# Performance work log

Hardware: AMD Instinct MI355X
Metric: run time of the kernel (lower is better)

## Reference

```python
import jax, jax.numpy as jnp
import numpy as np
import math

T_KER = 1.0
SIGMA = 0.1
COVAR = 5
EPS = 1e-6


def cos_kernel(a, b):
    # a:[B,N,D], b:[B,M,D] -> exp((cos_sim - 1)/T)
    num = jnp.einsum('bnd,bmd->bnm', a, b)
    den = jnp.linalg.norm(a, axis=-1)[..., None] * jnp.linalg.norm(b, axis=-1)[:, None] + EPS
    return jnp.exp((num / den - 1.0) / T_KER)


def get_local_cov(cov, K):
    # cov: [b,h,w,h,w] -> local KxK windows around the diagonal: [b,h,w,K*K]
    b, h, w = cov.shape[0], cov.shape[1], cov.shape[2]
    hw = h * w
    pad = K // 2
    covp = jnp.pad(cov, ((0, 0), (0, 0), (0, 0), (pad, pad), (pad, pad)))
    covp = covp.reshape(b, hw, h + K - 1, w + K - 1)
    dr, dc = np.meshgrid(np.arange(-pad, pad + 1), np.arange(-pad, pad + 1), indexing='ij')
    rb, cb = np.meshgrid(np.arange(pad, pad + h), np.arange(pad, pad + w), indexing='ij')
    rows = (rb[:, :, None, None] + dr[None, None]).reshape(hw, K * K)
    cols = (cb[:, :, None, None] + dc[None, None]).reshape(hw, K * K)
    pts = np.broadcast_to(np.arange(hw)[:, None], (hw, K * K))
    local = covp[:, pts, rows, cols]  # [b,hw,K*K]
    return local.reshape(b, h, w, K * K)


def reference(x, y, pos_w, pos_b):
    b, c, h1, w1 = x.shape
    h2, w2 = y.shape[2], y.shape[3]
    n2 = h2 * w2
    # positional encoding (fourier basis on [-1,1] grid)
    ys = jnp.linspace(-1 + 1 / h2, 1 - 1 / h2, h2)
    xs = jnp.linspace(-1 + 1 / w2, 1 - 1 / w2, w2)
    gy, gx = jnp.meshgrid(ys, xs, indexing='ij')
    coords = jnp.stack([gx, gy], axis=0)  # [2,h2,w2], (x,y) order
    f = jnp.cos(8 * math.pi * (jnp.einsum('dc,chw->dhw', pos_w, coords) + pos_b[:, None, None]))
    d = f.shape[0]
    xf = x.transpose(0, 2, 3, 1).reshape(b, h1 * w1, c)
    yf = y.transpose(0, 2, 3, 1).reshape(b, n2, c)
    ff = jnp.broadcast_to(f.transpose(1, 2, 0).reshape(1, n2, d), (b, n2, d))
    K_yy = cos_kernel(yf, yf)
    K_xy = cos_kernel(xf, yf)
    K_yy_plus = K_yy + SIGMA * jnp.eye(n2, dtype=K_yy.dtype)[None]
    I = jnp.broadcast_to(jnp.eye(n2, dtype=K_yy.dtype), (b, n2, n2))
    K_yy_inv = jnp.linalg.solve(K_yy_plus, I)
    mu = K_xy @ (K_yy_inv @ ff)  # [b, h1*w1, d]
    mu_x = mu.reshape(b, h1, w1, d).transpose(0, 3, 1, 2)
    K_xx = cos_kernel(xf, xf)
    cov = K_xx - K_xy @ (K_yy_inv @ jnp.swapaxes(K_xy, 1, 2))
    cov = cov.reshape(b, h1, w1, h1, w1)
    local = get_local_cov(cov, COVAR).transpose(0, 3, 1, 2)  # [b,K*K,h1,w1]
    return jnp.concatenate([mu_x, local], axis=1)


def setup_inputs() -> dict:
    key = jax.random.key(0)
    k0, k1, k2, k3 = jax.random.split(key, 4)
    return {
        'x': jax.random.normal(k0, (2, 512, 64, 64), dtype=jnp.float32),
        'y': jax.random.normal(k1, (2, 512, 64, 64), dtype=jnp.float32),
        'pos_w': jax.random.normal(k2, (64, 2), dtype=jnp.float32) * 0.5,
        'pos_b': jax.random.normal(k3, (64,), dtype=jnp.float32) * 0.1,
    }
```

## Files before the change

### kernel.cpp

```cpp
#include <hip/hip_runtime.h>
#include <math.h>

#define NPT 4096
#define CCH 512
#define NB 64
#define NKB 64
#define LDB 4160
#define SIGF 0.1f
#define CEPS 1e-6f
#define PI8 25.132741228718345f

#define APSTR ((size_t)2080 * 4096)
#define ILSTR ((size_t)64 * 4096)

typedef __attribute__((ext_vector_type(8))) short bf16x8;
typedef __attribute__((ext_vector_type(4))) float f32x4;
typedef __attribute__((ext_vector_type(4))) unsigned short us4;
typedef unsigned short ushort_t;

__device__ __forceinline__ size_t tbase(int I, int J) {
    return ((size_t)((I * (I + 1) >> 1) + J)) << 12;
}

__device__ inline ushort_t f2bf_rne(float x) {
    unsigned u = __float_as_uint(x);
    unsigned r = u + 0x7FFFu + ((u >> 16) & 1u);
    return (ushort_t)(r >> 16);
}
__device__ inline float bf2f(ushort_t h) { return __uint_as_float(((unsigned)h) << 16); }

__device__ inline void split4(float4 v, us4& h, us4& l) {
    h[0] = f2bf_rne(v.x); l[0] = f2bf_rne(v.x - bf2f(h[0]));
    h[1] = f2bf_rne(v.y); l[1] = f2bf_rne(v.y - bf2f(h[1]));
    h[2] = f2bf_rne(v.z); l[2] = f2bf_rne(v.z - bf2f(h[2]));
    h[3] = f2bf_rne(v.w); l[3] = f2bf_rne(v.w - bf2f(h[3]));
}

__global__ __launch_bounds__(256) void norms_kernel(const float* __restrict__ X,
                                                    float* __restrict__ nrm, int bofs) {
    int slot = blockIdx.y;
    int p = blockIdx.x * 256 + threadIdx.x;
    const float* Xb = X + (size_t)(slot + bofs) * CCH * NPT;
    float s = 0.f;
    #pragma unroll 8
    for (int ch = 0; ch < CCH; ++ch) {
        float v = Xb[(size_t)ch * NPT + p];
        s += v * v;
    }
    nrm[slot * NPT + p] = sqrtf(s);
}

__global__ __launch_bounds__(256) void split_kernel(const float* __restrict__ X,
                                                    ushort_t* __restrict__ Hi,
                                                    ushort_t* __restrict__ Lo,
                                                    int bofs) {
    int ch0 = blockIdx.x * 64, pt0 = blockIdx.y * 64;
    const float* Xb = X + (size_t)bofs * CCH * NPT;
    __shared__ float ls[64][65];
    int tid = threadIdx.x;
    for (int t = tid; t < 4096; t += 256) {
        int chl = t >> 6, ptl = t & 63;
        ls[chl][ptl] = Xb[(size_t)(ch0 + chl) * NPT + pt0 + ptl];
    }
    __syncthreads();
    for (int t = tid; t < 4096; t += 256) {
        int ptl = t >> 6, chl = t & 63;
        float v = ls[chl][ptl];
        ushort_t h = f2bf_rne(v);
        float lo = v - bf2f(h);
        Hi[(size_t)(pt0 + ptl) * CCH + ch0 + chl] = h;
        Lo[(size_t)(pt0 + ptl) * CCH + ch0 + chl] = f2bf_rne(lo);
    }
}

__global__ __launch_bounds__(256) void gramA_packed_kernel(
    const ushort_t* __restrict__ Yhi, const ushort_t* __restrict__ Ylo,
    const float* __restrict__ nY, float* __restrict__ Cp)
{
    int bx = blockIdx.x, by = blockIdx.y;
    if (bx > by) return;
    int bm = by * 128, bn = bx * 128;

    __shared__ __align__(16) ushort_t Ah[128][40];
    __shared__ __align__(16) ushort_t Al[128][40];
    __shared__ __align__(16) ushort_t Bh[128][40];
    __shared__ __align__(16) ushort_t Bl[128][40];

    int tid = threadIdx.x;
    int lane = tid & 63, wid = tid >> 6;
    int wr = wid >> 1, wc = wid & 1;

    f32x4 acc[4][4];
    #pragma unroll
    for (int i = 0; i < 4; ++i)
        #pragma unroll
        for (int j = 0; j < 4; ++j) acc[i][j] = (f32x4){0.f, 0.f, 0.f, 0.f};

    int arr = tid >> 6;
    int srow = lane >> 2, sc4 = lane & 3;
    const ushort_t* src = (arr == 0 || arr == 2) ? Yhi : Ylo;
    int pbase = (arr < 2) ? bm : bn;
    ushort_t* dst = (arr == 0) ? &Ah[0][0] : (arr == 1) ? &Al[0][0] : (arr == 2) ? &Bh[0][0] : &Bl[0][0];

    for (int k0 = 0; k0 < CCH; k0 += 32) {
        #pragma unroll
        for (int it = 0; it < 8; ++it) {
            int row = it * 16 + srow;
            const ushort_t* g = src + (size_t)(pbase + row) * CCH + k0 + sc4 * 8;
            bf16x8 v = *(const bf16x8*)g;
            *(bf16x8*)(dst + row * 40 + sc4 * 8) = v;
        }
        __syncthreads();
        bf16x8 afh[4], afl[4], bfh[4], bfl[4];
        int kcol = (lane >> 4) * 8;
        #pragma unroll
        for (int mi = 0; mi < 4; ++mi) {
            int r = wr * 64 + mi * 16 + (lane & 15);
            afh[mi] = *(const bf16x8*)&Ah[r][kcol];
            afl[mi] = *(const bf16x8*)&Al[r][kcol];
        }
        #pragma unroll
        for (int nj = 0; nj < 4; ++nj) {
            int r = wc * 64 + nj * 16 + (lane & 15);
            bfh[nj] = *(const bf16x8*)&Bh[r][kcol];
            bfl[nj] = *(const bf16x8*)&Bl[r][kcol];
        }
        #pragma unroll
        for (int mi = 0; mi < 4; ++mi)
            #pragma unroll
            for (int nj = 0; nj < 4; ++nj) {
                acc[mi][nj] = __builtin_amdgcn_mfma_f32_16x16x32_bf16(afh[mi], bfh[nj], acc[mi][nj], 0, 0, 0);
                acc[mi][nj] = __builtin_amdgcn_mfma_f32_16x16x32_bf16(afh[mi], bfl[nj], acc[mi][nj], 0, 0, 0);
                acc[mi][nj] = __builtin_amdgcn_mfma_f32_16x16x32_bf16(afl[mi], bfh[nj], acc[mi][nj], 0, 0, 0);
            }
        __syncthreads();
    }

    int I = (bm >> 6) + wr, J = (bn >> 6) + wc;
    if (J > I) return;
    float* Ct = Cp + tbase(I, J);
    #pragma unroll
    for (int nj = 0; nj < 4; ++nj) {
        int cin = nj * 16 + (lane & 15);
        float nbv = nY[bn + wc * 64 + cin];
        #pragma unroll
        for (int mi = 0; mi < 4; ++mi) {
            f32x4 a = acc[mi][nj];
            #pragma unroll
            for (int q = 0; q < 4; ++q) {
                int rin = mi * 16 + (lane >> 4) * 4 + q;
                float den = nY[bm + wr * 64 + rin] * nbv + CEPS;
                float v = expf(a[q] / den - 1.0f);
                if (I == J && rin == cin) v += SIGF;
                Ct[(rin << 6) + cin] = v;
            }
        }
    }
}

__global__ __launch_bounds__(256) void gramX_kernel(
    const ushort_t* __restrict__ Yhi, const ushort_t* __restrict__ Ylo,
    const float* __restrict__ Xf,
    const float* __restrict__ nY, const float* __restrict__ nX,
    float* __restrict__ Cm)
{
    int bm = blockIdx.y * 128, bn = blockIdx.x * 128;

    __shared__ __align__(16) ushort_t Ah[128][40];
    __shared__ __align__(16) ushort_t Al[128][40];
    __shared__ __align__(16) ushort_t Bh[128][40];
    __shared__ __align__(16) ushort_t Bl[128][40];

    int tid = threadIdx.x;
    int lane = tid & 63, wid = tid >> 6;
    int wr = wid >> 1, wc = wid & 1;

    f32x4 acc[4][4];
    #pragma unroll
    for (int i = 0; i < 4; ++i)
        #pragma unroll
        for (int j = 0; j < 4; ++j) acc[i][j] = (f32x4){0.f, 0.f, 0.f, 0.f};

    int srow = lane >> 2, sc4 = lane & 3;

    for (int k0 = 0; k0 < CCH; k0 += 32) {
        if (tid < 128) {
            const ushort_t* src = (tid < 64) ? Yhi : Ylo;
            ushort_t* dst = (tid < 64) ? &Ah[0][0] : &Al[0][0];
            #pragma unroll
            for (int it = 0; it < 8; ++it) {
                int row = it * 16 + srow;
                bf16x8 v = *(const bf16x8*)(src + (size_t)(bm + row) * CCH + k0 + sc4 * 8);
                *(bf16x8*)(dst + row * 40 + sc4 * 8) = v;
            }
        } else {
            int e0 = (tid - 128) * 8;
            #pragma unroll
            for (int i = 0; i < 8; ++i) {
                int e = e0 + i;
                int ch = e >> 5, p4 = e & 31;
                float4 v = *(const float4*)&Xf[(size_t)(k0 + ch) * NPT + bn + (p4 << 2)];
                us4 h, l;
                split4(v, h, l);
                #pragma unroll
                for (int q = 0; q < 4; ++q) {
                    Bh[(p4 << 2) + q][ch] = h[q];
                    Bl[(p4 << 2) + q][ch] = l[q];
                }
            }
        }
        __syncthreads();
        bf16x8 afh[4], afl[4], bfh[4], bfl[4];
        int kcol = (lane >> 4) * 8;
        #pragma unroll
        for (int mi = 0; mi < 4; ++mi) {
            int r = wr * 64 + mi * 16 + (lane & 15);
            afh[mi] = *(const bf16x8*)&Ah[r][kcol];
            afl[mi] = *(const bf16x8*)&Al[r][kcol];
        }
        #pragma unroll
        for (int nj = 0; nj < 4; ++nj) {
            int r = wc * 64 + nj * 16 + (lane & 15);
            bfh[nj] = *(const bf16x8*)&Bh[r][kcol];
            bfl[nj] = *(const bf16x8*)&Bl[r][kcol];
        }
        #pragma unroll
        for (int mi = 0; mi < 4; ++mi)
            #pragma unroll
            for (int nj = 0; nj < 4; ++nj) {
                acc[mi][nj] = __builtin_amdgcn_mfma_f32_16x16x32_bf16(afh[mi], bfh[nj], acc[mi][nj], 0, 0, 0);
                acc[mi][nj] = __builtin_amdgcn_mfma_f32_16x16x32_bf16(afh[mi], bfl[nj], acc[mi][nj], 0, 0, 0);
                acc[mi][nj] = __builtin_amdgcn_mfma_f32_16x16x32_bf16(afl[mi], bfh[nj], acc[mi][nj], 0, 0, 0);
            }
        __syncthreads();
    }

    #pragma unroll
    for (int nj = 0; nj < 4; ++nj) {
        int col = bn + wc * 64 + nj * 16 + (lane & 15);
        float nbv = nX[col];
        #pragma unroll
        for (int mi = 0; mi < 4; ++mi) {
            f32x4 a = acc[mi][nj];
            #pragma unroll
            for (int q = 0; q < 4; ++q) {
                int row = bm + wr * 64 + mi * 16 + (lane >> 4) * 4 + q;
                float den = nY[row] * nbv + CEPS;
                Cm[(size_t)row * LDB + col] = expf(a[q] / den - 1.0f);
            }
        }
    }
}

__global__ __launch_bounds__(256) void features_kernel(const float* __restrict__ pw,
                                                       const float* __restrict__ pb,
                                                       float* __restrict__ Brhs) {
    int g = blockIdx.x * 256 + threadIdx.x;
    int q = g >> 6, dd = g & 63;
    int hh = q >> 6, ww = q & 63;
    float gy = -1.0f + (2 * hh + 1) / 64.0f;
    float gx = -1.0f + (2 * ww + 1) / 64.0f;
    float ph = PI8 * (pw[dd * 2 + 0] * gx + pw[dd * 2 + 1] * gy + pb[dd]);
    Brhs[(size_t)q * LDB + NPT + dd] = cosf(ph);
}

__global__ __launch_bounds__(256) void potf2_packed_kernel(float* __restrict__ AmatP,
                                                           float* __restrict__ invL, int kb) {
    __shared__ float a[NB][NB + 4];
    __shared__ float iv[NB][NB + 4];
    __shared__ float ddiag[NB];
    int slot = blockIdx.z;
    float* Ab = AmatP + (size_t)slot * APSTR + tbase(kb, kb);
    int tid = threadIdx.x;
    int tx = tid & 15, ty = tid >> 4;
    for (int t = tid; t < NB * NB; t += 256) {
        int i = t >> 6, j = t & 63;
        a[i][j] = Ab[(i << 6) + j];
        iv[i][j] = 0.0f;
    }
    __syncthreads();
    for (int j = 0; j < NB; ++j) {
        float ajj = sqrtf(a[j][j]);
        float dinv = 1.0f / ajj;
        if (tid == 0) ddiag[j] = ajj;
        for (int i = j + 1 + tid; i < NB; i += 256) a[i][j] *= dinv;
        for (int c = tid; c <= j; c += 256)
            iv[j][c] = ((c == j ? 1.0f : 0.0f) - iv[j][c]) * dinv;
        __syncthreads();
        for (int i = j + 1 + ty; i < NB; i += 16) {
            float lij = a[i][j];
            for (int jj = j + 1 + tx; jj < NB; jj += 16)
                a[i][jj] -= lij * a[jj][j];
            for (int c = tx; c <= j; c += 16)
                iv[i][c] += lij * iv[j][c];
        }
        __syncthreads();
    }
    float* iL = invL + (size_t)slot * ILSTR + ((size_t)kb << 12);
    for (int t = tid; t < NB * NB; t += 256) {
        int i = t >> 6, j = t & 63;
        if (j < i)       Ab[(i << 6) + j] = a[i][j];
        else if (j == i) Ab[(i << 6) + j] = ddiag[i];
        iL[t] = (j <= i) ? iv[i][j] : 0.0f;
    }
}

__global__ __launch_bounds__(256) void trsm_packed_kernel(float* __restrict__ AmatP,
                                                          const float* __restrict__ invL, int kb) {
    int slot = blockIdx.z;
    int I = kb + 1 + blockIdx.x;
    float* At = AmatP + (size_t)slot * APSTR + tbase(I, kb);
    const float* iL = invL + (size_t)slot * ILSTR + ((size_t)kb << 12);

    __shared__ __align__(16) ushort_t Aoh[64][72], Aol[64][72];
    __shared__ __align__(16) ushort_t Bh[64][72], Bl[64][72];

    int tid = threadIdx.x, lane = tid & 63, w = tid >> 6;
    int frow = lane & 15, fk = (lane >> 4) << 3;
    f32x4 acc[4];
    #pragma unroll
    for (int j = 0; j < 4; ++j) acc[j] = (f32x4){0, 0, 0, 0};

    for (int e = tid; e < 1024; e += 256) {
        int r = e >> 4, k4 = e & 15;
        us4 h, l;
        float4 v = *(const float4*)&At[(r << 6) + (k4 << 2)];
        split4(v, h, l);
        *(us4*)&Aoh[r][k4 << 2] = h; *(us4*)&Aol[r][k4 << 2] = l;
        float4 u = *(const float4*)&iL[(r << 6) + (k4 << 2)];
        split4(u, h, l);
        *(us4*)&Bh[r][k4 << 2] = h; *(us4*)&Bl[r][k4 << 2] = l;
    }
    __syncthreads();
    #pragma unroll
    for (int kk0 = 0; kk0 < 64; kk0 += 32) {
        bf16x8 ah = *(const bf16x8*)&Aoh[(w << 4) + frow][kk0 + fk];
        bf16x8 al = *(const bf16x8*)&Aol[(w << 4) + frow][kk0 + fk];
        #pragma unroll
        for (int nj = 0; nj < 4; ++nj) {
            bf16x8 bh = *(const bf16x8*)&Bh[(nj << 4) + frow][kk0 + fk];
            bf16x8 bl = *(const bf16x8*)&Bl[(nj << 4) + frow][kk0 + fk];
            acc[nj] = __builtin_amdgcn_mfma_f32_16x16x32_bf16(ah, bh, acc[nj], 0, 0, 0);
            acc[nj] = __builtin_amdgcn_mfma_f32_16x16x32_bf16(ah, bl, acc[nj], 0, 0, 0);
            acc[nj] = __builtin_amdgcn_mfma_f32_16x16x32_bf16(al, bh, acc[nj], 0, 0, 0);
        }
    }
    #pragma unroll
    for (int nj = 0; nj < 4; ++nj)
        #pragma unroll
        for (int q = 0; q < 4; ++q) {
            int rin = (w << 4) + ((lane >> 4) << 2) + q;
            At[(rin << 6) + (nj << 4) + frow] = acc[nj][q];
        }
}

__global__ __launch_bounds__(256) void syrk_fact_packed_kernel(float* __restrict__ AmatP,
                                                               float* __restrict__ invL, int kb) {
    int bi = blockIdx.y, bj = blockIdx.x;
    if (bj > bi) return;
    int slot = blockIdx.z;
    int I = kb + 1 + bi, J = kb + 1 + bj;
    float* base = AmatP + (size_t)slot * APSTR;
    const float* Pi_t = base + tbase(I, kb);
    const float* Pj_t = base + tbase(J, kb);
    float* Ct = base + tbase(I, J);

    __shared__ __align__(16) char smem[36864];
    ushort_t (*Pih)[72] = (ushort_t(*)[72])(smem);
    ushort_t (*Pil)[72] = (ushort_t(*)[72])(smem + 9216);
    ushort_t (*Pjh)[72] = (ushort_t(*)[72])(smem + 18432);
    ushort_t (*Pjl)[72] = (ushort_t(*)[72])(smem + 27648);
    float (*fa)[68] = (float(*)[68])(smem);
    float (*fiv)[68] = (float(*)[68])(smem + 17408);
    float* fdd = (float*)(smem + 34816);

    int tid = threadIdx.x, lane = tid & 63, w = tid >> 6;
    int frow = lane & 15, fk = (lane >> 4) << 3;
    f32x4 acc[4];
    #pragma unroll
    for (int j = 0; j < 4; ++j) acc[j] = (f32x4){0, 0, 0, 0};

    for (int e = tid; e < 1024; e += 256) {
        int r = e >> 4, k4 = e & 15;
        us4 h, l;
        float4 v = *(const float4*)&Pi_t[(r << 6) + (k4 << 2)];
        split4(v, h, l);
        *(us4*)&Pih[r][k4 << 2] = h; *(us4*)&Pil[r][k4 << 2] = l;
        float4 u = *(const float4*)&Pj_t[(r << 6) + (k4 << 2)];
        split4(u, h, l);
        *(us4*)&Pjh[r][k4 << 2] = h; *(us4*)&Pjl[r][k4 << 2] = l;
    }
    __syncthreads();
    #pragma unroll
    for (int kk0 = 0; kk0 < 64; kk0 += 32) {
        bf16x8 ah = *(const bf16x8*)&Pih[(w << 4) + frow][kk0 + fk];
        bf16x8 al = *(const bf16x8*)&Pil[(w << 4) + frow][kk0 + fk];
        #pragma unroll
        for (int nj = 0; nj < 4; ++nj) {
            bf16x8 bh = *(const bf16x8*)&Pjh[(nj << 4) + frow][kk0 + fk];
            bf16x8 bl = *(const bf16x8*)&Pjl[(nj << 4) + frow][kk0 + fk];
            acc[nj] = __builtin_amdgcn_mfma_f32_16x16x32_bf16(ah, bh, acc[nj], 0, 0, 0);
            acc[nj] = __builtin_amdgcn_mfma_f32_16x16x32_bf16(ah, bl, acc[nj], 0, 0, 0);
            acc[nj] = __builtin_amdgcn_mfma_f32_16x16x32_bf16(al, bh, acc[nj], 0, 0, 0);
        }
    }

    if (!(bi == 0 && bj == 0)) {
        #pragma unroll
        for (int nj = 0; nj < 4; ++nj) {
            int cin = (nj << 4) + frow;
            #pragma unroll
            for (int q = 0; q < 4; ++q) {
                int rin = (w << 4) + ((lane >> 4) << 2) + q;
                Ct[(rin << 6) + cin] -= acc[nj][q];
            }
        }
        return;
    }

    __syncthreads();
    #pragma unroll
    for (int nj = 0; nj < 4; ++nj) {
        int cin = (nj << 4) + frow;
        #pragma unroll
        for (int q = 0; q < 4; ++q) {
            int rin = (w << 4) + ((lane >> 4) << 2) + q;
            fa[rin][cin] = Ct[(rin << 6) + cin] - acc[nj][q];
            fiv[rin][cin] = 0.0f;
        }
    }
    __syncthreads();
    int tx = tid & 15, ty = tid >> 4;
    for (int j = 0; j < NB; ++j) {
        float ajj = sqrtf(fa[j][j]);
        float dinv = 1.0f / ajj;
        if (tid == 0) fdd[j] = ajj;
        for (int i = j + 1 + tid; i < NB; i += 256) fa[i][j] *= dinv;
        for (int c = tid; c <= j; c += 256)
            fiv[j][c] = ((c == j ? 1.0f : 0.0f) - fiv[j][c]) * dinv;
        __syncthreads();
        for (int i = j + 1 + ty; i < NB; i += 16) {
            float lij = fa[i][j];
            for (int jj = j + 1 + tx; jj < NB; jj += 16)
                fa[i][jj] -= lij * fa[jj][j];
            for (int c = tx; c <= j; c += 16)
                fiv[i][c] += lij * fiv[j][c];
        }
        __syncthreads();
    }
    float* iL = invL + (size_t)slot * ILSTR + ((size_t)(kb + 1) << 12);
    for (int t = tid; t < NB * NB; t += 256) {
        int i = t >> 6, j = t & 63;
        if (j < i)       Ct[(i << 6) + j] = fa[i][j];
        else if (j == i) Ct[(i << 6) + j] = fdd[i];
        iL[t] = (j <= i) ? fiv[i][j] : 0.0f;
    }
}

__global__ __launch_bounds__(256) void trsm_rhs_kernel(float* __restrict__ Brhs,
                                                       const float* __restrict__ invL) {
    int n0 = blockIdx.x * 64;
    __shared__ float invLs[64][68];
    __shared__ float Tds[64][68];
    int tid = threadIdx.x;
    for (int e = tid; e < 1024; e += 256) {
        int r = e >> 4, k4 = e & 15;
        float4 v = *(const float4*)&Brhs[(size_t)r * LDB + n0 + (k4 << 2)];
        int c = k4 << 2;
        Tds[r][c] = v.x; Tds[r][c + 1] = v.y; Tds[r][c + 2] = v.z; Tds[r][c + 3] = v.w;
        float4 u = *(const float4*)&invL[(r << 6) + (k4 << 2)];
        invLs[r][c] = u.x; invLs[r][c + 1] = u.y; invLs[r][c + 2] = u.z; invLs[r][c + 3] = u.w;
    }
    __syncthreads();
    int col = tid & 63, rg = tid >> 6;
    #pragma unroll
    for (int i = 0; i < 16; ++i) {
        int r = (i << 2) + rg;
        float s = 0.f;
        #pragma unroll 16
        for (int k = 0; k < 64; ++k) s += invLs[r][k] * Tds[k][col];
        Brhs[(size_t)r * LDB + n0 + col] = s;
    }
}

__global__ __launch_bounds__(256) void solve_step_kernel(const float* __restrict__ AmatP,
                                                         float* __restrict__ Brhs,
                                                         const float* __restrict__ invL, int kb) {
    int n0 = blockIdx.x * 64;
    int I = kb + 1 + blockIdx.y;
    int rb = kb * NB;
    int ri = I * NB;
    const float* Lt = AmatP + tbase(I, kb);

    __shared__ __align__(16) char smem[36864];
    ushort_t (*Lh)[72] = (ushort_t(*)[72])(smem);
    ushort_t (*Ll)[72] = (ushort_t(*)[72])(smem + 9216);
    ushort_t (*Uh)[72] = (ushort_t(*)[72])(smem + 18432);
    ushort_t (*Ul)[72] = (ushort_t(*)[72])(smem + 27648);
    float (*invLs)[68] = (float(*)[68])(smem);
    float (*Tds)[68]   = (float(*)[68])(smem + 18432);

    int tid = threadIdx.x, lane = tid & 63, w = tid >> 6;
    int frow = lane & 15, fk = (lane >> 4) << 3;

    for (int e = tid; e < 1024; e += 256) {
        int r = e >> 4, k4 = e & 15;
        us4 h, l;
        float4 v = *(const float4*)&Lt[(r << 6) + (k4 << 2)];
        split4(v, h, l);
        *(us4*)&Lh[r][k4 << 2] = h; *(us4*)&Ll[r][k4 << 2] = l;
        float4 u = *(const float4*)&Brhs[(size_t)(rb + r) * LDB + n0 + (k4 << 2)];
        split4(u, h, l);
        #pragma unroll
        for (int q = 0; q < 4; ++q) {
            Uh[(k4 << 2) + q][r] = h[q];
            Ul[(k4 << 2) + q][r] = l[q];
        }
    }
    __syncthreads();

    f32x4 acc[4];
    #pragma unroll
    for (int j = 0; j < 4; ++j) acc[j] = (f32x4){0, 0, 0, 0};
    #pragma unroll
    for (int kk0 = 0; kk0 < 64; kk0 += 32) {
        bf16x8 ah = *(const bf16x8*)&Lh[(w << 4) + frow][kk0 + fk];
        bf16x8 al = *(const bf16x8*)&Ll[(w << 4) + frow][kk0 + fk];
        #pragma unroll
        for (int nj = 0; nj < 4; ++nj) {
            bf16x8 bh = *(const bf16x8*)&Uh[(nj << 4) + frow][kk0 + fk];
            bf16x8 bl = *(const bf16x8*)&Ul[(nj << 4) + frow][kk0 + fk];
            acc[nj] = __builtin_amdgcn_mfma_f32_16x16x32_bf16(ah, bh, acc[nj], 0, 0, 0);
            acc[nj] = __builtin_amdgcn_mfma_f32_16x16x32_bf16(ah, bl, acc[nj], 0, 0, 0);
            acc[nj] = __builtin_amdgcn_mfma_f32_16x16x32_bf16(al, bh, acc[nj], 0, 0, 0);
        }
    }

    if (blockIdx.y > 0) {
        #pragma unroll
        for (int nj = 0; nj < 4; ++nj) {
            int cin = (nj << 4) + frow;
            #pragma unroll
            for (int q = 0; q < 4; ++q) {
                int rin = (w << 4) + ((lane >> 4) << 2) + q;
                Brhs[(size_t)(ri + rin) * LDB + n0 + cin] -= acc[nj][q];
            }
        }
        return;
    }

    __syncthreads();
    #pragma unroll
    for (int nj = 0; nj < 4; ++nj) {
        int cin = (nj << 4) + frow;
        #pragma unroll
        for (int q = 0; q < 4; ++q) {
            int rin = (w << 4) + ((lane >> 4) << 2) + q;
            Tds[rin][cin] = Brhs[(size_t)(ri + rin) * LDB + n0 + cin] - acc[nj][q];
        }
    }
    const float* iL = invL + ((size_t)(kb + 1) << 12);
    for (int e = tid; e < 1024; e += 256) {
        int r = e >> 4, k4 = e & 15;
        float4 u = *(const float4*)&iL[(r << 6) + (k4 << 2)];
        int c = k4 << 2;
        invLs[r][c] = u.x; invLs[r][c + 1] = u.y; invLs[r][c + 2] = u.z; invLs[r][c + 3] = u.w;
    }
    __syncthreads();
    int col = tid & 63, rg = tid >> 6;
    #pragma unroll
    for (int i = 0; i < 16; ++i) {
        int r = (i << 2) + rg;
        float s = 0.f;
        #pragma unroll 16
        for (int k = 0; k < 64; ++k) s += invLs[r][k] * Tds[k][col];
        Brhs[(size_t)(ri + r) * LDB + n0 + col] = s;
    }
}

__global__ __launch_bounds__(256) void mu_kernel(const float* __restrict__ Brhs,
                                                 float* __restrict__ out, int bofs) {
    const float* Bb = Brhs;
    int p0 = blockIdx.x * 64;
    __shared__ float Us[16][65];
    __shared__ float Vs[16][65];
    float acc[4][4] = {};
    int tid = threadIdx.x, tx = tid & 15, ty = tid >> 4;
    for (int q0 = 0; q0 < NPT; q0 += 16) {
        for (int t = tid; t < 1024; t += 256) {
            int kk = t >> 6, c = t & 63;
            Us[kk][c] = Bb[(size_t)(q0 + kk) * LDB + p0 + c];
            Vs[kk][c] = Bb[(size_t)(q0 + kk) * LDB + NPT + c];
        }
        __syncthreads();
        #pragma unroll
        for (int kk = 0; kk < 16; ++kk) {
            float uv[4], vv[4];
            #pragma unroll
            for (int i = 0; i < 4; ++i) { uv[i] = Us[kk][ty * 4 + i]; vv[i] = Vs[kk][tx * 4 + i]; }
            #pragma unroll
            for (int i = 0; i < 4; ++i)
                #pragma unroll
                for (int j = 0; j < 4; ++j) acc[i][j] += uv[i] * vv[j];
        }
        __syncthreads();
    }
    #pragma unroll
    for (int i = 0; i < 4; ++i)
        #pragma unroll
        for (int j = 0; j < 4; ++j)
            out[((size_t)bofs * 89 + tx * 4 + j) * NPT + p0 + ty * 4 + i] = acc[i][j];
}

__global__ __launch_bounds__(256) void kxx_local_kernel(const float* __restrict__ X,
                                                        const float* __restrict__ nxb,
                                                        float* __restrict__ tmp, int bofs) {
    int r = blockIdx.y;
    int c0 = blockIdx.x * 16;
    const float* Xb = X + (size_t)bofs * CCH * NPT;
    __shared__ float Xs[32][104];
    int tid = threadIdx.x;
    int t0 = tid, t1 = tid + 256;
    int pl0 = t0 / 25, jj0 = t0 % 25;
    int pl1 = t1 / 25, jj1 = t1 % 25;
    int pidx0 = 40 + pl0 + 2;
    int jidx0 = (jj0 / 5) * 20 + pl0 + (jj0 % 5);
    int pidx1 = 40 + pl1 + 2;
    int jidx1 = (jj1 / 5) * 20 + pl1 + (jj1 % 5);
    float acc0 = 0.f, acc1 = 0.f;
    for (int ch0 = 0; ch0 < CCH; ch0 += 32) {
        for (int t = tid; t < 32 * 100; t += 256) {
            int ch = t / 100, i = t % 100;
            int s = i / 20, cc = i % 20;
            int gr = r + s - 2, gc = c0 - 2 + cc;
            float v = 0.f;
            if (gr >= 0 && gr < 64 && gc >= 0 && gc < 64)
                v = Xb[(size_t)(ch0 + ch) * NPT + gr * 64 + gc];
            Xs[ch][i] = v;
        }
        __syncthreads();
        #pragma unroll 8
        for (int kk = 0; kk < 32; ++kk) {
            acc0 += Xs[kk][pidx0] * Xs[kk][jidx0];
            if (t1 < 400) acc1 += Xs[kk][pidx1] * Xs[kk][jidx1];
        }
        __syncthreads();
    }
    {
        int p = r * 64 + c0 + pl0;
        int qr = r + jj0 / 5 - 2, qc = c0 + pl0 + jj0 % 5 - 2;
        float v = 0.f;
        if (qr >= 0 && qr < 64 && qc >= 0 && qc < 64) {
            int q = qr * 64 + qc;
            v = expf(acc0 / (nxb[p] * nxb[q] + CEPS) - 1.0f);
        }
        tmp[(size_t)jj0 * NPT + p] = v;
    }
    if (t1 < 400) {
        int p = r * 64 + c0 + pl1;
        int qr = r + jj1 / 5 - 2, qc = c0 + pl1 + jj1 % 5 - 2;
        float v = 0.f;
        if (qr >= 0 && qr < 64 && qc >= 0 && qc < 64) {
            int q = qr * 64 + qc;
            v = expf(acc1 / (nxb[p] * nxb[q] + CEPS) - 1.0f);
        }
        tmp[(size_t)jj1 * NPT + p] = v;
    }
}

__global__ __launch_bounds__(256) void cov_local_kernel(const float* __restrict__ Brhs,
                                                        const float* __restrict__ tmp,
                                                        float* __restrict__ out, int bofs) {
    int r = blockIdx.y;
    int c0 = blockIdx.x * 16;
    const float* Ub = Brhs;
    __shared__ float Us[64][104];
    int tid = threadIdx.x;
    int t0 = tid, t1 = tid + 256;
    int pl0 = t0 / 25, jj0 = t0 % 25;
    int pl1 = t1 / 25, jj1 = t1 % 25;
    int pidx0 = 40 + pl0 + 2;
    int jidx0 = (jj0 / 5) * 20 + pl0 + (jj0 % 5);
    int pidx1 = 40 + pl1 + 2;
    int jidx1 = (jj1 / 5) * 20 + pl1 + (jj1 % 5);
    float acc0 = 0.f, acc1 = 0.f;
    for (int q0 = 0; q0 < NPT; q0 += 64) {
        for (int t = tid; t < 64 * 100; t += 256) {
            int qq = t / 100, i = t % 100;
            int s = i / 20, cc = i % 20;
            int gr = r + s - 2, gc = c0 - 2 + cc;
            float v = 0.f;
            if (gr >= 0 && gr < 64 && gc >= 0 && gc < 64)
                v = Ub[(size_t)(q0 + qq) * LDB + gr * 64 + gc];
            Us[qq][i] = v;
        }
        __syncthreads();
        #pragma unroll 8
        for (int kk = 0; kk < 64; ++kk) {
            acc0 += Us[kk][pidx0] * Us[kk][jidx0];
            if (t1 < 400) acc1 += Us[kk][pidx1] * Us[kk][jidx1];
        }
        __syncthreads();
    }
    {
        int p = r * 64 + c0 + pl0;
        int qr = r + jj0 / 5 - 2, qc = c0 + pl0 + jj0 % 5 - 2;
        float v = 0.f;
        if (qr >= 0 && qr < 64 && qc >= 0 && qc < 64)
            v = tmp[(size_t)jj0 * NPT + p] - acc0;
        out[((size_t)bofs * 89 + 64 + jj0) * NPT + p] = v;
    }
    if (t1 < 400) {
        int p = r * 64 + c0 + pl1;
        int qr = r + jj1 / 5 - 2, qc = c0 + pl1 + jj1 % 5 - 2;
        float v = 0.f;
        if (qr >= 0 && qr < 64 && qc >= 0 && qc < 64)
            v = tmp[(size_t)jj1 * NPT + p] - acc1;
        out[((size_t)bofs * 89 + 64 + jj1) * NPT + p] = v;
    }
}

extern "C" void kernel_launch(void* const* d_in, const int* in_sizes, int n_in,
                              void* d_out, int out_size, void* d_ws, size_t ws_size,
                              hipStream_t stream) {
    (void)in_sizes; (void)n_in; (void)out_size;
    const float* x  = (const float*)d_in[0];
    const float* y  = (const float*)d_in[1];
    const float* pw = (const float*)d_in[2];
    const float* pb = (const float*)d_in[3];
    float* out = (float*)d_out;
    float* ws  = (float*)d_ws;

    const size_t NEED = 2 * APSTR + (size_t)NPT * LDB + 2 * ILSTR + 4 * NPT + 2 * ((size_t)NPT * CCH / 2);
    if (ws_size < NEED * sizeof(float)) return;

    float* AmatP = ws;
    float* Brhs  = AmatP + 2 * APSTR;
    float* invL  = Brhs + (size_t)NPT * LDB;
    float* nx    = invL + 2 * ILSTR;
    float* ny    = nx + 2 * NPT;
    float* ysBuf = ny + 2 * NPT;
    ushort_t* ysH = (ushort_t*)ysBuf;
    ushort_t* ysL = ysH + (size_t)NPT * CCH;
    float* tmp = invL;

    norms_kernel<<<dim3(16, 2), 256, 0, stream>>>(x, nx, 0);
    norms_kernel<<<dim3(16, 2), 256, 0, stream>>>(y, ny, 0);

    for (int b = 0; b < 2; ++b) {
        split_kernel<<<dim3(8, 64, 1), 256, 0, stream>>>(y, ysH, ysL, b);
        gramA_packed_kernel<<<dim3(32, 32, 1), 256, 0, stream>>>(
            ysH, ysL, ny + (size_t)b * NPT, AmatP + (size_t)b * APSTR);
    }

    potf2_packed_kernel<<<dim3(1, 1, 2), 256, 0, stream>>>(AmatP, invL, 0);
    for (int kb = 0; kb < NKB - 1; ++kb) {
        int nt = NKB - 1 - kb;
        trsm_packed_kernel<<<dim3(nt, 1, 2), 256, 0, stream>>>(AmatP, invL, kb);
        syrk_fact_packed_kernel<<<dim3(nt, nt, 2), 256, 0, stream>>>(AmatP, invL, kb);
    }

    for (int b = 0; b < 2; ++b) {
        split_kernel<<<dim3(8, 64, 1), 256, 0, stream>>>(y, ysH, ysL, b);
        features_kernel<<<dim3(1024, 1), 256, 0, stream>>>(pw, pb, Brhs);
        gramX_kernel<<<dim3(32, 32, 1), 256, 0, stream>>>(
            ysH, ysL, x + (size_t)b * CCH * NPT, ny + (size_t)b * NPT, nx + (size_t)b * NPT, Brhs);

        trsm_rhs_kernel<<<dim3(65, 1, 1), 256, 0, stream>>>(Brhs, invL + (size_t)b * ILSTR);
        for (int kb = 0; kb < NKB - 1; ++kb) {
            solve_step_kernel<<<dim3(65, NKB - 1 - kb, 1), 256, 0, stream>>>(
                AmatP + (size_t)b * APSTR, Brhs, invL + (size_t)b * ILSTR, kb);
        }

        mu_kernel<<<dim3(64, 1, 1), 256, 0, stream>>>(Brhs, out, b);
        kxx_local_kernel<<<dim3(4, 64, 1), 256, 0, stream>>>(x, nx + (size_t)b * NPT, tmp, b);
        cov_local_kernel<<<dim3(4, 64, 1), 256, 0, stream>>>(Brhs, tmp, out, b);
    }
}
```

Before: 11.39 ms.

## Batch triangular solves across both batches and split local covariance reduction

```diff
diff --git a/kernel.cpp b/kernel.cpp
--- a/kernel.cpp
+++ b/kernel.cpp
@@ -106,8 +106,7 @@
         #pragma unroll
         for (int it = 0; it < 8; ++it) {
             int row = it * 16 + srow;
-            const ushort_t* g = src + (size_t)(pbase + row) * CCH + k0 + sc4 * 8;
-            bf16x8 v = *(const bf16x8*)g;
+            bf16x8 v = *(const bf16x8*)(src + (size_t)(pbase + row) * CCH + k0 + sc4 * 8);
             *(bf16x8*)(dst + row * 40 + sc4 * 8) = v;
         }
         __syncthreads();
@@ -458,17 +457,21 @@
 }
 
 __global__ __launch_bounds__(256) void trsm_rhs_kernel(float* __restrict__ Brhs,
-                                                       const float* __restrict__ invL) {
+                                                       const float* __restrict__ invL,
+                                                       size_t brStride) {
+    int slot = blockIdx.z;
+    float* Bb = Brhs + (size_t)slot * brStride;
+    const float* iL = invL + (size_t)slot * ILSTR;
     int n0 = blockIdx.x * 64;
     __shared__ float invLs[64][68];
     __shared__ float Tds[64][68];
     int tid = threadIdx.x;
     for (int e = tid; e < 1024; e += 256) {
         int r = e >> 4, k4 = e & 15;
-        float4 v = *(const float4*)&Brhs[(size_t)r * LDB + n0 + (k4 << 2)];
+        float4 v = *(const float4*)&Bb[(size_t)r * LDB + n0 + (k4 << 2)];
         int c = k4 << 2;
         Tds[r][c] = v.x; Tds[r][c + 1] = v.y; Tds[r][c + 2] = v.z; Tds[r][c + 3] = v.w;
-        float4 u = *(const float4*)&invL[(r << 6) + (k4 << 2)];
+        float4 u = *(const float4*)&iL[(r << 6) + (k4 << 2)];
         invLs[r][c] = u.x; invLs[r][c + 1] = u.y; invLs[r][c + 2] = u.z; invLs[r][c + 3] = u.w;
     }
     __syncthreads();
@@ -479,18 +482,22 @@
         float s = 0.f;
         #pragma unroll 16
         for (int k = 0; k < 64; ++k) s += invLs[r][k] * Tds[k][col];
-        Brhs[(size_t)r * LDB + n0 + col] = s;
+        Bb[(size_t)r * LDB + n0 + col] = s;
     }
 }
 
 __global__ __launch_bounds__(256) void solve_step_kernel(const float* __restrict__ AmatP,
                                                          float* __restrict__ Brhs,
-                                                         const float* __restrict__ invL, int kb) {
+                                                         const float* __restrict__ invL,
+                                                         size_t brStride, int kb) {
+    int slot = blockIdx.z;
     int n0 = blockIdx.x * 64;
     int I = kb + 1 + blockIdx.y;
     int rb = kb * NB;
     int ri = I * NB;
-    const float* Lt = AmatP + tbase(I, kb);
+    const float* Lt = AmatP + (size_t)slot * APSTR + tbase(I, kb);
+    const float* iLbase = invL + (size_t)slot * ILSTR;
+    float* Bb = Brhs + (size_t)slot * brStride;
 
     __shared__ __align__(16) char smem[36864];
     ushort_t (*Lh)[72] = (ushort_t(*)[72])(smem);
@@ -509,7 +516,7 @@
         float4 v = *(const float4*)&Lt[(r << 6) + (k4 << 2)];
         split4(v, h, l);
         *(us4*)&Lh[r][k4 << 2] = h; *(us4*)&Ll[r][k4 << 2] = l;
-        float4 u = *(const float4*)&Brhs[(size_t)(rb + r) * LDB + n0 + (k4 << 2)];
+        float4 u = *(const float4*)&Bb[(size_t)(rb + r) * LDB + n0 + (k4 << 2)];
         split4(u, h, l);
         #pragma unroll
         for (int q = 0; q < 4; ++q) {
@@ -543,7 +550,7 @@
             #pragma unroll
             for (int q = 0; q < 4; ++q) {
                 int rin = (w << 4) + ((lane >> 4) << 2) + q;
-                Brhs[(size_t)(ri + rin) * LDB + n0 + cin] -= acc[nj][q];
+                Bb[(size_t)(ri + rin) * LDB + n0 + cin] -= acc[nj][q];
             }
         }
         return;
@@ -556,13 +563,13 @@
         #pragma unroll
         for (int q = 0; q < 4; ++q) {
             int rin = (w << 4) + ((lane >> 4) << 2) + q;
-            Tds[rin][cin] = Brhs[(size_t)(ri + rin) * LDB + n0 + cin] - acc[nj][q];
-        }
-    }
-    const float* iL = invL + ((size_t)(kb + 1) << 12);
+            Tds[rin][cin] = Bb[(size_t)(ri + rin) * LDB + n0 + cin] - acc[nj][q];
+        }
+    }
+    const float* iL2 = iLbase + ((size_t)(kb + 1) << 12);
     for (int e = tid; e < 1024; e += 256) {
         int r = e >> 4, k4 = e & 15;
-        float4 u = *(const float4*)&iL[(r << 6) + (k4 << 2)];
+        float4 u = *(const float4*)&iL2[(r << 6) + (k4 << 2)];
         int c = k4 << 2;
         invLs[r][c] = u.x; invLs[r][c + 1] = u.y; invLs[r][c + 2] = u.z; invLs[r][c + 3] = u.w;
     }
@@ -574,7 +581,7 @@
         float s = 0.f;
         #pragma unroll 16
         for (int k = 0; k < 64; ++k) s += invLs[r][k] * Tds[k][col];
-        Brhs[(size_t)(ri + r) * LDB + n0 + col] = s;
+        Bb[(size_t)(ri + r) * LDB + n0 + col] = s;
     }
 }
 
@@ -610,6 +617,11 @@
         #pragma unroll
         for (int j = 0; j < 4; ++j)
             out[((size_t)bofs * 89 + tx * 4 + j) * NPT + p0 + ty * 4 + i] = acc[i][j];
+}
+
+__global__ __launch_bounds__(256) void zero_kernel(float* __restrict__ p, int n) {
+    int i = blockIdx.x * 256 + threadIdx.x;
+    if (i < n) p[i] = 0.0f;
 }
 
 __global__ __launch_bounds__(256) void kxx_local_kernel(const float* __restrict__ X,
@@ -668,11 +680,11 @@
     }
 }
 
-__global__ __launch_bounds__(256) void cov_local_kernel(const float* __restrict__ Brhs,
-                                                        const float* __restrict__ tmp,
-                                                        float* __restrict__ out, int bofs) {
+__global__ __launch_bounds__(256) void cov_part_kernel(const float* __restrict__ Brhs,
+                                                       float* __restrict__ covAcc) {
     int r = blockIdx.y;
     int c0 = blockIdx.x * 16;
+    int ks = blockIdx.z;
     const float* Ub = Brhs;
     __shared__ float Us[64][104];
     int tid = threadIdx.x;
@@ -684,7 +696,8 @@
     int pidx1 = 40 + pl1 + 2;
     int jidx1 = (jj1 / 5) * 20 + pl1 + (jj1 % 5);
     float acc0 = 0.f, acc1 = 0.f;
-    for (int q0 = 0; q0 < NPT; q0 += 64) {
+    int qbeg = ks * 512, qend = qbeg + 512;
+    for (int q0 = qbeg; q0 < qend; q0 += 64) {
         for (int t = tid; t < 64 * 100; t += 256) {
             int qq = t / 100, i = t % 100;
             int s = i / 20, cc = i % 20;
@@ -704,20 +717,25 @@
     }
     {
         int p = r * 64 + c0 + pl0;
-        int qr = r + jj0 / 5 - 2, qc = c0 + pl0 + jj0 % 5 - 2;
-        float v = 0.f;
-        if (qr >= 0 && qr < 64 && qc >= 0 && qc < 64)
-            v = tmp[(size_t)jj0 * NPT + p] - acc0;
-        out[((size_t)bofs * 89 + 64 + jj0) * NPT + p] = v;
+        atomicAdd(&covAcc[(size_t)jj0 * NPT + p], acc0);
     }
     if (t1 < 400) {
         int p = r * 64 + c0 + pl1;
-        int qr = r + jj1 / 5 - 2, qc = c0 + pl1 + jj1 % 5 - 2;
-        float v = 0.f;
-        if (qr >= 0 && qr < 64 && qc >= 0 && qc < 64)
-            v = tmp[(size_t)jj1 * NPT + p] - acc1;
-        out[((size_t)bofs * 89 + 64 + jj1) * NPT + p] = v;
-    }
+        atomicAdd(&covAcc[(size_t)jj1 * NPT + p], acc1);
+    }
+}
+
+__global__ __launch_bounds__(256) void cov_finish_kernel(const float* __restrict__ tmpX,
+                                                         const float* __restrict__ covAcc,
+                                                         float* __restrict__ out, int bofs) {
+    int e = blockIdx.x * 256 + threadIdx.x;
+    int jj = e >> 12, p = e & 4095;
+    int r = p >> 6, c = p & 63;
+    int qr = r + jj / 5 - 2, qc = c + jj % 5 - 2;
+    float v = 0.f;
+    if (qr >= 0 && qr < 64 && qc >= 0 && qc < 64)
+        v = tmpX[e] - covAcc[e];
+    out[((size_t)bofs * 89 + 64 + jj) * NPT + p] = v;
 }
 
 extern "C" void kernel_launch(void* const* d_in, const int* in_sizes, int n_in,
@@ -731,18 +749,20 @@
     float* out = (float*)d_out;
     float* ws  = (float*)d_ws;
 
-    const size_t NEED = 2 * APSTR + (size_t)NPT * LDB + 2 * ILSTR + 4 * NPT + 2 * ((size_t)NPT * CCH / 2);
-    if (ws_size < NEED * sizeof(float)) return;
+    const size_t SZ_B = (size_t)NPT * LDB;
+    const size_t NEED1 = 2 * APSTR + SZ_B + 2 * ILSTR + 4 * NPT + (size_t)NPT * CCH;
+    const size_t NEED2 = NEED1 + SZ_B;
+    if (ws_size < NEED1 * sizeof(float)) return;
+    int twoB = (ws_size >= NEED2 * sizeof(float)) ? 1 : 0;
 
     float* AmatP = ws;
     float* Brhs  = AmatP + 2 * APSTR;
-    float* invL  = Brhs + (size_t)NPT * LDB;
+    float* invL  = Brhs + (size_t)(twoB ? 2 : 1) * SZ_B;
     float* nx    = invL + 2 * ILSTR;
     float* ny    = nx + 2 * NPT;
     float* ysBuf = ny + 2 * NPT;
     ushort_t* ysH = (ushort_t*)ysBuf;
     ushort_t* ysL = ysH + (size_t)NPT * CCH;
-    float* tmp = invL;
 
     norms_kernel<<<dim3(16, 2), 256, 0, stream>>>(x, nx, 0);
     norms_kernel<<<dim3(16, 2), 256, 0, stream>>>(y, ny, 0);
@@ -760,20 +780,47 @@
         syrk_fact_packed_kernel<<<dim3(nt, nt, 2), 256, 0, stream>>>(AmatP, invL, kb);
     }
 
-    for (int b = 0; b < 2; ++b) {
-        split_kernel<<<dim3(8, 64, 1), 256, 0, stream>>>(y, ysH, ysL, b);
-        features_kernel<<<dim3(1024, 1), 256, 0, stream>>>(pw, pb, Brhs);
-        gramX_kernel<<<dim3(32, 32, 1), 256, 0, stream>>>(
-            ysH, ysL, x + (size_t)b * CCH * NPT, ny + (size_t)b * NPT, nx + (size_t)b * NPT, Brhs);
-
-        trsm_rhs_kernel<<<dim3(65, 1, 1), 256, 0, stream>>>(Brhs, invL + (size_t)b * ILSTR);
+    if (twoB) {
+        for (int b = 0; b < 2; ++b) {
+            split_kernel<<<dim3(8, 64, 1), 256, 0, stream>>>(y, ysH, ysL, b);
+            features_kernel<<<dim3(1024, 1), 256, 0, stream>>>(pw, pb, Brhs + (size_t)b * SZ_B);
+            gramX_kernel<<<dim3(32, 32, 1), 256, 0, stream>>>(
+                ysH, ysL, x + (size_t)b * CCH * NPT, ny + (size_t)b * NPT, nx + (size_t)b * NPT,
+                Brhs + (size_t)b * SZ_B);
+        }
+        trsm_rhs_kernel<<<dim3(65, 1, 2), 256, 0, stream>>>(Brhs, invL, SZ_B);
         for (int kb = 0; kb < NKB - 1; ++kb) {
-            solve_step_kernel<<<dim3(65, NKB - 1 - kb, 1), 256, 0, stream>>>(
-                AmatP + (size_t)b * APSTR, Brhs, invL + (size_t)b * ILSTR, kb);
-        }
-
-        mu_kernel<<<dim3(64, 1, 1), 256, 0, stream>>>(Brhs, out, b);
-        kxx_local_kernel<<<dim3(4, 64, 1), 256, 0, stream>>>(x, nx + (size_t)b * NPT, tmp, b);
-        cov_local_kernel<<<dim3(4, 64, 1), 256, 0, stream>>>(Brhs, tmp, out, b);
-    }
-}
+            solve_step_kernel<<<dim3(65, NKB - 1 - kb, 2), 256, 0, stream>>>(
+                AmatP, Brhs, invL, SZ_B, kb);
+        }
+        for (int b = 0; b < 2; ++b) {
+            float* Bb = Brhs + (size_t)b * SZ_B;
+            float* covAcc = invL + (size_t)b * ILSTR;
+            float* tmpX   = covAcc + (size_t)25 * NPT;
+            zero_kernel<<<dim3(400), 256, 0, stream>>>(covAcc, 25 * NPT);
+            mu_kernel<<<dim3(64, 1, 1), 256, 0, stream>>>(Bb, out, b);
+            kxx_local_kernel<<<dim3(4, 64, 1), 256, 0, stream>>>(x, nx + (size_t)b * NPT, tmpX, b);
+            cov_part_kernel<<<dim3(4, 64, 8), 256, 0, stream>>>(Bb, covAcc);
+            cov_finish_kernel<<<dim3(400), 256, 0, stream>>>(tmpX, covAcc, out, b);
+        }
+    } else {
+        for (int b = 0; b < 2; ++b) {
+            split_kernel<<<dim3(8, 64, 1), 256, 0, stream>>>(y, ysH, ysL, b);
+            features_kernel<<<dim3(1024, 1), 256, 0, stream>>>(pw, pb, Brhs);
+            gramX_kernel<<<dim3(32, 32, 1), 256, 0, stream>>>(
+                ysH, ysL, x + (size_t)b * CCH * NPT, ny + (size_t)b * NPT, nx + (size_t)b * NPT, Brhs);
+            trsm_rhs_kernel<<<dim3(65, 1, 1), 256, 0, stream>>>(Brhs, invL + (size_t)b * ILSTR, 0);
+            for (int kb = 0; kb < NKB - 1; ++kb) {
+                solve_step_kernel<<<dim3(65, NKB - 1 - kb, 1), 256, 0, stream>>>(
+                    AmatP + (size_t)b * APSTR, Brhs, invL + (size_t)b * ILSTR, 0, kb);
+            }
+            float* covAcc = invL + (size_t)b * ILSTR;
+            float* tmpX   = covAcc + (size_t)25 * NPT;
+            zero_kernel<<<dim3(400), 256, 0, stream>>>(covAcc, 25 * NPT);
+            mu_kernel<<<dim3(64, 1, 1), 256, 0, stream>>>(Brhs, out, b);
+            kxx_local_kernel<<<dim3(4, 64, 1), 256, 0, stream>>>(x, nx + (size_t)b * NPT, tmpX, b);
+            cov_part_kernel<<<dim3(4, 64, 8), 256, 0, stream>>>(Brhs, covAcc);
+            cov_finish_kernel<<<dim3(400), 256, 0, stream>>>(tmpX, covAcc, out, b);
+        }
+    }
+}
```

Measured after the change: 10.01 ms. 12.2% less time.
